# Kernel optimization log

Measured on AMD Instinct MI355X. Metric: run time of the kernel, lower is better.

Reference implementation:

```python
import jax, jax.numpy as jnp
import numpy as np

NEG_INF = -1.0e9  # matches the module's explicit -1e9 masking constant


def setup_inputs() -> dict:
    key = jax.random.key(0)
    B, T, D = 8, 2048, 1024
    x = jax.random.normal(key, (B, T, D), dtype=jnp.float32)
    return {"x": x}


def reference(x):
    # x: [B, T, D]
    T = x.shape[1]
    # raw QK^T scores: [B, T, T]
    scores = jnp.einsum('btd,bsd->bts', x, x)
    # torch.tril(scores, -1) + torch.triu(ones*-1e9, 0):
    # keep strictly-lower entries, set diagonal and upper to -1e9.
    strict_lower = jnp.tril(jnp.ones((T, T), dtype=bool), k=-1)
    scores = jnp.where(strict_lower, scores, jnp.float32(NEG_INF))
    # NOTE: row 0 is all -1e9 -> softmax yields uniform 1/T (faithful to the torch code).
    att_weights = jax.nn.softmax(scores, axis=-1)  # [B, T, T]
    att_vec = jnp.einsum('bts,bsd->btd', att_weights, x)  # [B, T, D]
    return att_vec, att_weights
```

## Files before the change

### kernel.cpp

```cpp
#include <hip/hip_runtime.h>

#define B_ 8
#define T_ 2048
#define D_ 1024

typedef __attribute__((ext_vector_type(8))) short bf16x8;
typedef __attribute__((ext_vector_type(8))) _Float16 f16x8;
typedef __attribute__((ext_vector_type(4))) float f32x4;
typedef __attribute__((ext_vector_type(8))) unsigned short u16x8;
typedef __attribute__((ext_vector_type(4))) unsigned short u16x4;

__device__ __forceinline__ unsigned short f2bf(float f) {
  union { float f; unsigned u; } v; v.f = f;
  unsigned r = v.u + 0x7FFFu + ((v.u >> 16) & 1u);
  return (unsigned short)(r >> 16);
}
__device__ __forceinline__ float bf2f(unsigned short h) {
  union { unsigned u; float f; } v; v.u = ((unsigned)h) << 16; return v.f;
}
__device__ __forceinline__ unsigned short f2h(float f) {
  union { _Float16 h; unsigned short u; } v; v.h = (_Float16)f; return v.u;
}

__device__ __forceinline__ void gl2lds16(const void* g, void* l) {
  __builtin_amdgcn_global_load_lds(
      (__attribute__((address_space(1))) void*)g,
      (__attribute__((address_space(3))) void*)l, 16, 0, 0);
}

__global__ __launch_bounds__(256) void prep_kernel(
    const float* __restrict__ x,
    unsigned short* __restrict__ xh, unsigned short* __restrict__ xl,
    unsigned short* __restrict__ xth) {
  const int b = blockIdx.z;
  const int t0 = blockIdx.y << 6;
  const int d0 = blockIdx.x << 6;
  __shared__ unsigned short tf[64][68];
  const int tid = threadIdx.x;
  const int r = tid >> 2, cq = tid & 3;
  const size_t xoff = ((size_t)b * T_ + t0 + r) * D_ + d0;
#pragma unroll
  for (int k = 0; k < 4; ++k) {
    const int col = (cq << 2) + (k << 4);
    const float4 v = *(const float4*)(x + xoff + col);
    const unsigned short h0 = f2bf(v.x), h1 = f2bf(v.y), h2 = f2bf(v.z), h3 = f2bf(v.w);
    const unsigned short l0 = f2bf(v.x - bf2f(h0)), l1 = f2bf(v.y - bf2f(h1));
    const unsigned short l2 = f2bf(v.z - bf2f(h2)), l3 = f2bf(v.w - bf2f(h3));
    u16x4 hv = {h0, h1, h2, h3}, lv = {l0, l1, l2, l3};
    *(u16x4*)(xh + xoff + col) = hv;
    *(u16x4*)(xl + xoff + col) = lv;
    tf[col + 0][r] = f2h(v.x); tf[col + 1][r] = f2h(v.y);
    tf[col + 2][r] = f2h(v.z); tf[col + 3][r] = f2h(v.w);
  }
  __syncthreads();
  const int dr = tid >> 2, tq = tid & 3;
  const size_t toff = ((size_t)b * D_ + d0 + dr) * T_ + t0;
#pragma unroll
  for (int c = 0; c < 2; ++c) {
    const int tcol = (tq << 3) + (c << 5);
    *(u16x8*)(xth + toff + tcol) = *(const u16x8*)&tf[dr][tcol];
  }
}

__global__ __launch_bounds__(256, 4) void scores_mfma(
    const unsigned short* __restrict__ xh, const unsigned short* __restrict__ xl,
    float* __restrict__ w) {
  const int id = blockIdx.x;
  const int sid = ((id & 7) * 136) + (id >> 3);
  const int b = sid / 136;
  const int L = sid - b * 136;
  int tt = (int)((sqrtf(8.f * (float)L + 1.f) - 1.f) * 0.5f);
  while (((tt + 1) * (tt + 2) >> 1) <= L) ++tt;
  while (((tt * (tt + 1)) >> 1) > L) --tt;
  const int ts = L - ((tt * (tt + 1)) >> 1);

  const int t0 = tt << 7, s0 = ts << 7;
  __shared__ unsigned short Ah[128 * 32];
  __shared__ unsigned short Al[128 * 32];
  __shared__ unsigned short Bh[128 * 32];
  __shared__ unsigned short Bl[128 * 32];
  const int tid = threadIdx.x;
  const int lane = tid & 63, wv = tid >> 6;
  const int wr = (wv >> 1) << 6, wc = (wv & 1) << 6;
  const int quad = lane >> 4, r16 = lane & 15;
  const int swz = ((quad ^ (r16 & 3) ^ ((r16 >> 2) & 1)) << 3);
  const size_t xb = (size_t)b * T_ * D_;

  f32x4 acc[4][4];
#pragma unroll
  for (int i = 0; i < 4; ++i)
#pragma unroll
    for (int j = 0; j < 4; ++j) acc[i][j] = (f32x4){0.f, 0.f, 0.f, 0.f};

  for (int k0 = 0; k0 < D_; k0 += 32) {
    __syncthreads();
#pragma unroll
    for (int i = 0; i < 2; ++i) {
      const int cc = (wv << 7) + (i << 6) + lane;
      const int row = cc >> 2, q = cc & 3;
      const int gq = q ^ (row & 3) ^ ((row >> 2) & 1);
      const int ldsoff = (((wv << 7) + (i << 6)) << 3);
      const size_t ga = xb + (size_t)(t0 + row) * D_ + k0 + (gq << 3);
      const size_t gb = xb + (size_t)(s0 + row) * D_ + k0 + (gq << 3);
      gl2lds16(xh + ga, &Ah[ldsoff]);
      gl2lds16(xl + ga, &Al[ldsoff]);
      gl2lds16(xh + gb, &Bh[ldsoff]);
      gl2lds16(xl + gb, &Bl[ldsoff]);
    }
    __syncthreads();
    bf16x8 ah[4], al[4];
#pragma unroll
    for (int i = 0; i < 4; ++i) {
      const int ra = ((wr + (i << 4) + r16) << 5) + swz;
      ah[i] = *(const bf16x8*)&Ah[ra];
      al[i] = *(const bf16x8*)&Al[ra];
    }
#pragma unroll
    for (int j = 0; j < 4; ++j) {
      const int rb = ((wc + (j << 4) + r16) << 5) + swz;
      const bf16x8 bhj = *(const bf16x8*)&Bh[rb];
      const bf16x8 blj = *(const bf16x8*)&Bl[rb];
#pragma unroll
      for (int i = 0; i < 4; ++i)
        acc[i][j] = __builtin_amdgcn_mfma_f32_16x16x32_bf16(ah[i], bhj, acc[i][j], 0, 0, 0);
#pragma unroll
      for (int i = 0; i < 4; ++i)
        acc[i][j] = __builtin_amdgcn_mfma_f32_16x16x32_bf16(ah[i], blj, acc[i][j], 0, 0, 0);
#pragma unroll
      for (int i = 0; i < 4; ++i)
        acc[i][j] = __builtin_amdgcn_mfma_f32_16x16x32_bf16(al[i], bhj, acc[i][j], 0, 0, 0);
    }
  }

  float* wb = w + (size_t)b * T_ * T_;
#pragma unroll
  for (int i = 0; i < 4; ++i)
#pragma unroll
    for (int j = 0; j < 4; ++j) {
      const int rr = t0 + wr + (i << 4) + (quad << 2);
      const int cc = s0 + wc + (j << 4) + r16;
#pragma unroll
      for (int rg = 0; rg < 4; ++rg)
        wb[(size_t)(rr + rg) * T_ + cc] = acc[i][j][rg];
    }
}

template <bool EMIT>
__global__ __launch_bounds__(256) void softmax_kernel(float* __restrict__ w,
                                                      unsigned short* __restrict__ wf) {
  const int row = (blockIdx.x << 2) + (threadIdx.x >> 6);
  const int t = row & (T_ - 1);
  const int lane = threadIdx.x & 63;
  float* wr = w + (size_t)row * T_;
  unsigned short* wfr = wf + (size_t)row * T_;

  if (t == 0) {
    const float u = 1.0f / 2048.0f;
    const float4 uv = {u, u, u, u};
#pragma unroll
    for (int k = 0; k < 8; ++k) *(float4*)&wr[(lane << 2) + (k << 8)] = uv;
    if (EMIT && lane < 32) {
      u16x4 z = {0, 0, 0, 0};
      *(u16x4*)&wfr[lane << 2] = z;
    }
    return;
  }

  float4 v[8];
  float m = -3.0e38f;
#pragma unroll
  for (int k = 0; k < 8; ++k) {
    const int s = (lane << 2) + (k << 8);
    float4 val = {-1.0e30f, -1.0e30f, -1.0e30f, -1.0e30f};
    if (s < t) {
      const float4 g = *(const float4*)&wr[s];
      val.x = g.x;
      val.y = (s + 1 < t) ? g.y : -1.0e30f;
      val.z = (s + 2 < t) ? g.z : -1.0e30f;
      val.w = (s + 3 < t) ? g.w : -1.0e30f;
    }
    v[k] = val;
    m = fmaxf(m, fmaxf(fmaxf(val.x, val.y), fmaxf(val.z, val.w)));
  }
#pragma unroll
  for (int off = 32; off; off >>= 1) m = fmaxf(m, __shfl_xor(m, off));

  float l = 0.f;
#pragma unroll
  for (int k = 0; k < 8; ++k) {
    v[k].x = __expf(v[k].x - m);
    v[k].y = __expf(v[k].y - m);
    v[k].z = __expf(v[k].z - m);
    v[k].w = __expf(v[k].w - m);
    l += (v[k].x + v[k].y) + (v[k].z + v[k].w);
  }
#pragma unroll
  for (int off = 32; off; off >>= 1) l += __shfl_xor(l, off);
  const float inv = 1.0f / l;

  const int smax_emit = ((t >> 7) + 1) << 7;
#pragma unroll
  for (int k = 0; k < 8; ++k) {
    const int s = (lane << 2) + (k << 8);
    const float4 o = {v[k].x * inv, v[k].y * inv, v[k].z * inv, v[k].w * inv};
    *(float4*)&wr[s] = o;
    if (EMIT && s < smax_emit) {
      u16x4 h = {f2h(o.x), f2h(o.y), f2h(o.z), f2h(o.w)};
      *(u16x4*)&wfr[s] = h;
    }
  }
}

template <bool USE_WF16>
__global__ __launch_bounds__(256, 4) void av_mfma(
    const float* __restrict__ w, const unsigned short* __restrict__ wf,
    const unsigned short* __restrict__ xth, float* __restrict__ out) {
  const int xid = blockIdx.x;
  const int td = xid >> 4;
  const int ti = xid & 15;
  const int tt = (ti < 8) ? ti : (23 - ti);
  const int b = blockIdx.z;
  const int t0 = tt << 7, d0 = td << 7;
  __shared__ unsigned short Aw[128 * 64];
  __shared__ unsigned short Bx[128 * 64];
  const int tid = threadIdx.x;
  const int lane = tid & 63, wv = tid >> 6;
  const int wr = (wv >> 1) << 6, wc = (wv & 1) << 6;
  const int quad = lane >> 4, r16 = lane & 15;
  const size_t xtb = (size_t)b * D_ * T_;
  const size_t wbase = (size_t)b * T_ * T_;
  const int smax = t0 + 128;

  f32x4 acc[4][4];
#pragma unroll
  for (int i = 0; i < 4; ++i)
#pragma unroll
    for (int j = 0; j < 4; ++j) acc[i][j] = (f32x4){0.f, 0.f, 0.f, 0.f};

  for (int s0 = 0; s0 < smax; s0 += 64) {
    __syncthreads();
    if (USE_WF16) {
#pragma unroll
      for (int i = 0; i < 4; ++i) {
        const int cc = (wv << 8) + (i << 6) + lane;
        const int rowa = cc >> 3, q = cc & 7;
        const int gq = q ^ (rowa & 7);
        const int ldsoff = (((wv << 8) + (i << 6)) << 3);
        gl2lds16(wf + wbase + (size_t)(t0 + rowa) * T_ + s0 + (gq << 3), &Aw[ldsoff]);
      }
    } else {
      const int rowa = tid >> 1, half = tid & 1;
      const float* g = w + wbase + (size_t)(t0 + rowa) * T_ + s0 + (half << 5);
      const int rs = rowa & 7;
#pragma unroll
      for (int p = 0; p < 4; ++p) {
        const float4 va = ((const float4*)g)[2 * p];
        const float4 vb = ((const float4*)g)[2 * p + 1];
        u16x8 pk = {f2h(va.x), f2h(va.y), f2h(va.z), f2h(va.w),
                    f2h(vb.x), f2h(vb.y), f2h(vb.z), f2h(vb.w)};
        const int c = (half << 2) + p;
        *(u16x8*)&Aw[(rowa << 6) + ((c ^ rs) << 3)] = pk;
      }
    }
#pragma unroll
    for (int i = 0; i < 4; ++i) {
      const int cc = (wv << 8) + (i << 6) + lane;
      const int rowb = cc >> 3, q = cc & 7;
      const int gq = q ^ (rowb & 7);
      const int ldsoff = (((wv << 8) + (i << 6)) << 3);
      gl2lds16(xth + xtb + (size_t)(d0 + rowb) * T_ + s0 + (gq << 3), &Bx[ldsoff]);
    }
    __syncthreads();
#pragma unroll
    for (int h = 0; h < 2; ++h) {
      f16x8 a[4];
#pragma unroll
      for (int i = 0; i < 4; ++i) {
        const int ar = wr + (i << 4) + r16;
        a[i] = *(const f16x8*)&Aw[(ar << 6) + ((((h << 2) | quad) ^ (ar & 7)) << 3)];
      }
#pragma unroll
      for (int j = 0; j < 4; ++j) {
        const int br = wc + (j << 4) + r16;
        const f16x8 bbj = *(const f16x8*)&Bx[(br << 6) + ((((h << 2) | quad) ^ (br & 7)) << 3)];
#pragma unroll
        for (int i = 0; i < 4; ++i)
          acc[i][j] = __builtin_amdgcn_mfma_f32_16x16x32_f16(a[i], bbj, acc[i][j], 0, 0, 0);
      }
    }
  }

  float* ob = out + (size_t)b * T_ * D_;
#pragma unroll
  for (int i = 0; i < 4; ++i)
#pragma unroll
    for (int j = 0; j < 4; ++j) {
      const int rr = t0 + wr + (i << 4) + (quad << 2);
      const int cc = d0 + wc + (j << 4) + r16;
#pragma unroll
      for (int rg = 0; rg < 4; ++rg)
        ob[(size_t)(rr + rg) * D_ + cc] = acc[i][j][rg];
    }
}

__global__ __launch_bounds__(256) void row0_partial(const float* __restrict__ x,
                                                    float* __restrict__ part) {
  const int tc = blockIdx.x, b = blockIdx.y;
  const int tid = threadIdx.x;
  const float* xb = x + ((size_t)b * T_ + (tc << 5)) * D_;
  float4 s = {0.f, 0.f, 0.f, 0.f};
#pragma unroll 4
  for (int r = 0; r < 32; ++r) {
    const float4 v = *(const float4*)(xb + (size_t)r * D_ + (tid << 2));
    s.x += v.x; s.y += v.y; s.z += v.z; s.w += v.w;
  }
  *(float4*)(part + ((size_t)((b << 6) + tc)) * D_ + (tid << 2)) = s;
}

__global__ __launch_bounds__(256) void row0_reduce(const float* __restrict__ part,
                                                   float* __restrict__ out) {
  const int b = blockIdx.x;
  const int tid = threadIdx.x;
  float4 s = {0.f, 0.f, 0.f, 0.f};
#pragma unroll 8
  for (int p = 0; p < 64; ++p) {
    const float4 v = *(const float4*)(part + ((size_t)((b << 6) + p)) * D_ + (tid << 2));
    s.x += v.x; s.y += v.y; s.z += v.z; s.w += v.w;
  }
  const float sc = 1.0f / 2048.0f;
  float4 o = {s.x * sc, s.y * sc, s.z * sc, s.w * sc};
  *(float4*)(out + (size_t)b * T_ * D_ + (tid << 2)) = o;
}

extern "C" void kernel_launch(void* const* d_in, const int* in_sizes, int n_in,
                              void* d_out, int out_size, void* d_ws, size_t ws_size,
                              hipStream_t stream) {
  const float* x = (const float*)d_in[0];
  float* att_vec = (float*)d_out;
  float* w = (float*)d_out + (size_t)B_ * T_ * D_;

  unsigned short* xh = (unsigned short*)att_vec;
  unsigned short* xl = xh + (size_t)B_ * T_ * D_;
  const size_t xthN = (size_t)B_ * D_ * T_;
  const size_t wfN = (size_t)B_ * T_ * T_;
  unsigned short* xth = (unsigned short*)d_ws;
  unsigned short* wf16 = xth + xthN;
  const size_t need = xthN * 2 + wfN * 2 + (size_t)512 * D_ * 4;
  const bool use_wf16 = (ws_size >= need);
  float* part = use_wf16 ? (float*)(wf16 + wfN) : (float*)(xth + xthN);

  prep_kernel<<<dim3(D_ / 64, T_ / 64, B_), 256, 0, stream>>>(x, xh, xl, xth);
  scores_mfma<<<dim3(8 * 136), 256, 0, stream>>>(xh, xl, w);
  if (use_wf16) {
    softmax_kernel<true><<<dim3(B_ * T_ / 4), 256, 0, stream>>>(w, wf16);
    av_mfma<true><<<dim3(128, 1, B_), 256, 0, stream>>>(w, wf16, xth, att_vec);
  } else {
    softmax_kernel<false><<<dim3(B_ * T_ / 4), 256, 0, stream>>>(w, wf16);
    av_mfma<false><<<dim3(128, 1, B_), 256, 0, stream>>>(w, wf16, xth, att_vec);
  }
  row0_partial<<<dim3(64, B_), 256, 0, stream>>>(x, part);
  row0_reduce<<<dim3(B_), 256, 0, stream>>>(part, att_vec);
}
```

Measured before the change: 505.6 us.

## Fuse row-0 column sums into prep, pair AV tiles, use nontemporal stores

```diff
diff --git a/kernel.cpp b/kernel.cpp
--- a/kernel.cpp
+++ b/kernel.cpp
@@ -21,6 +21,9 @@
 __device__ __forceinline__ unsigned short f2h(float f) {
   union { _Float16 h; unsigned short u; } v; v.h = (_Float16)f; return v.u;
 }
+__device__ __forceinline__ float h2f(unsigned short u) {
+  union { unsigned short u; _Float16 h; } v; v.u = u; return (float)v.h;
+}
 
 __device__ __forceinline__ void gl2lds16(const void* g, void* l) {
   __builtin_amdgcn_global_load_lds(
@@ -31,7 +34,7 @@
 __global__ __launch_bounds__(256) void prep_kernel(
     const float* __restrict__ x,
     unsigned short* __restrict__ xh, unsigned short* __restrict__ xl,
-    unsigned short* __restrict__ xth) {
+    unsigned short* __restrict__ xth, float* __restrict__ part) {
   const int b = blockIdx.z;
   const int t0 = blockIdx.y << 6;
   const int d0 = blockIdx.x << 6;
@@ -55,11 +58,19 @@
   __syncthreads();
   const int dr = tid >> 2, tq = tid & 3;
   const size_t toff = ((size_t)b * D_ + d0 + dr) * T_ + t0;
+  float cs = 0.f;
 #pragma unroll
   for (int c = 0; c < 2; ++c) {
     const int tcol = (tq << 3) + (c << 5);
-    *(u16x8*)(xth + toff + tcol) = *(const u16x8*)&tf[dr][tcol];
-  }
+    const u16x8 vv = *(const u16x8*)&tf[dr][tcol];
+    *(u16x8*)(xth + toff + tcol) = vv;
+#pragma unroll
+    for (int e = 0; e < 8; ++e) cs += h2f(vv[e]);
+  }
+  cs += __shfl_xor(cs, 1);
+  cs += __shfl_xor(cs, 2);
+  if (tq == 0)
+    part[(((size_t)b << 5) + blockIdx.y) * D_ + d0 + dr] = cs;
 }
 
 __global__ __launch_bounds__(256, 4) void scores_mfma(
@@ -156,9 +167,10 @@
 
   if (t == 0) {
     const float u = 1.0f / 2048.0f;
-    const float4 uv = {u, u, u, u};
-#pragma unroll
-    for (int k = 0; k < 8; ++k) *(float4*)&wr[(lane << 2) + (k << 8)] = uv;
+    const f32x4 uv = {u, u, u, u};
+#pragma unroll
+    for (int k = 0; k < 8; ++k)
+      __builtin_nontemporal_store(uv, (f32x4*)&wr[(lane << 2) + (k << 8)]);
     if (EMIT && lane < 32) {
       u16x4 z = {0, 0, 0, 0};
       *(u16x4*)&wfr[lane << 2] = z;
@@ -202,10 +214,10 @@
 #pragma unroll
   for (int k = 0; k < 8; ++k) {
     const int s = (lane << 2) + (k << 8);
-    const float4 o = {v[k].x * inv, v[k].y * inv, v[k].z * inv, v[k].w * inv};
-    *(float4*)&wr[s] = o;
+    const f32x4 o = {v[k].x * inv, v[k].y * inv, v[k].z * inv, v[k].w * inv};
+    __builtin_nontemporal_store(o, (f32x4*)&wr[s]);
     if (EMIT && s < smax_emit) {
-      u16x4 h = {f2h(o.x), f2h(o.y), f2h(o.z), f2h(o.w)};
+      u16x4 h = {f2h(o[0]), f2h(o[1]), f2h(o[2]), f2h(o[3])};
       *(u16x4*)&wfr[s] = h;
     }
   }
@@ -216,11 +228,10 @@
     const float* __restrict__ w, const unsigned short* __restrict__ wf,
     const unsigned short* __restrict__ xth, float* __restrict__ out) {
   const int xid = blockIdx.x;
-  const int td = xid >> 4;
-  const int ti = xid & 15;
-  const int tt = (ti < 8) ? ti : (23 - ti);
+  const int td = xid >> 3;
+  const int kp = xid & 7;
   const int b = blockIdx.z;
-  const int t0 = tt << 7, d0 = td << 7;
+  const int d0 = td << 7;
   __shared__ unsigned short Aw[128 * 64];
   __shared__ unsigned short Bx[128 * 64];
   const int tid = threadIdx.x;
@@ -229,92 +240,84 @@
   const int quad = lane >> 4, r16 = lane & 15;
   const size_t xtb = (size_t)b * D_ * T_;
   const size_t wbase = (size_t)b * T_ * T_;
-  const int smax = t0 + 128;
-
-  f32x4 acc[4][4];
-#pragma unroll
-  for (int i = 0; i < 4; ++i)
-#pragma unroll
-    for (int j = 0; j < 4; ++j) acc[i][j] = (f32x4){0.f, 0.f, 0.f, 0.f};
-
-  for (int s0 = 0; s0 < smax; s0 += 64) {
-    __syncthreads();
-    if (USE_WF16) {
+  float* ob = out + (size_t)b * T_ * D_;
+
+#pragma unroll 1
+  for (int mtile = 0; mtile < 2; ++mtile) {
+    const int tt = mtile ? (15 - kp) : kp;
+    const int t0 = tt << 7;
+    const int smax = t0 + 128;
+
+    f32x4 acc[4][4];
+#pragma unroll
+    for (int i = 0; i < 4; ++i)
+#pragma unroll
+      for (int j = 0; j < 4; ++j) acc[i][j] = (f32x4){0.f, 0.f, 0.f, 0.f};
+
+    for (int s0 = 0; s0 < smax; s0 += 64) {
+      __syncthreads();
+      if (USE_WF16) {
+#pragma unroll
+        for (int i = 0; i < 4; ++i) {
+          const int cc = (wv << 8) + (i << 6) + lane;
+          const int rowa = cc >> 3, q = cc & 7;
+          const int gq = q ^ (rowa & 7);
+          const int ldsoff = (((wv << 8) + (i << 6)) << 3);
+          gl2lds16(wf + wbase + (size_t)(t0 + rowa) * T_ + s0 + (gq << 3), &Aw[ldsoff]);
+        }
+      } else {
+        const int rowa = tid >> 1, half = tid & 1;
+        const float* g = w + wbase + (size_t)(t0 + rowa) * T_ + s0 + (half << 5);
+        const int rs = rowa & 7;
+#pragma unroll
+        for (int p = 0; p < 4; ++p) {
+          const float4 va = ((const float4*)g)[2 * p];
+          const float4 vb = ((const float4*)g)[2 * p + 1];
+          u16x8 pk = {f2h(va.x), f2h(va.y), f2h(va.z), f2h(va.w),
+                      f2h(vb.x), f2h(vb.y), f2h(vb.z), f2h(vb.w)};
+          const int c = (half << 2) + p;
+          *(u16x8*)&Aw[(rowa << 6) + ((c ^ rs) << 3)] = pk;
+        }
+      }
 #pragma unroll
       for (int i = 0; i < 4; ++i) {
         const int cc = (wv << 8) + (i << 6) + lane;
-        const int rowa = cc >> 3, q = cc & 7;
-        const int gq = q ^ (rowa & 7);
+        const int rowb = cc >> 3, q = cc & 7;
+        const int gq = q ^ (rowb & 7);
         const int ldsoff = (((wv << 8) + (i << 6)) << 3);
-        gl2lds16(wf + wbase + (size_t)(t0 + rowa) * T_ + s0 + (gq << 3), &Aw[ldsoff]);
+        gl2lds16(xth + xtb + (size_t)(d0 + rowb) * T_ + s0 + (gq << 3), &Bx[ldsoff]);
       }
-    } else {
-      const int rowa = tid >> 1, half = tid & 1;
-      const float* g = w + wbase + (size_t)(t0 + rowa) * T_ + s0 + (half << 5);
-      const int rs = rowa & 7;
-#pragma unroll
-      for (int p = 0; p < 4; ++p) {
-        const float4 va = ((const float4*)g)[2 * p];
-        const float4 vb = ((const float4*)g)[2 * p + 1];
-        u16x8 pk = {f2h(va.x), f2h(va.y), f2h(va.z), f2h(va.w),
-                    f2h(vb.x), f2h(vb.y), f2h(vb.z), f2h(vb.w)};
-        const int c = (half << 2) + p;
-        *(u16x8*)&Aw[(rowa << 6) + ((c ^ rs) << 3)] = pk;
+      __syncthreads();
+#pragma unroll
+      for (int h = 0; h < 2; ++h) {
+        f16x8 a[4];
+#pragma unroll
+        for (int i = 0; i < 4; ++i) {
+          const int ar = wr + (i << 4) + r16;
+          a[i] = *(const f16x8*)&Aw[(ar << 6) + ((((h << 2) | quad) ^ (ar & 7)) << 3)];
+        }
+#pragma unroll
+        for (int j = 0; j < 4; ++j) {
+          const int br = wc + (j << 4) + r16;
+          const f16x8 bbj = *(const f16x8*)&Bx[(br << 6) + ((((h << 2) | quad) ^ (br & 7)) << 3)];
+#pragma unroll
+          for (int i = 0; i < 4; ++i)
+            acc[i][j] = __builtin_amdgcn_mfma_f32_16x16x32_f16(a[i], bbj, acc[i][j], 0, 0, 0);
+        }
       }
     }
-#pragma unroll
-    for (int i = 0; i < 4; ++i) {
-      const int cc = (wv << 8) + (i << 6) + lane;
-      const int rowb = cc >> 3, q = cc & 7;
-      const int gq = q ^ (rowb & 7);
-      const int ldsoff = (((wv << 8) + (i << 6)) << 3);
-      gl2lds16(xth + xtb + (size_t)(d0 + rowb) * T_ + s0 + (gq << 3), &Bx[ldsoff]);
-    }
-    __syncthreads();
-#pragma unroll
-    for (int h = 0; h < 2; ++h) {
-      f16x8 a[4];
-#pragma unroll
-      for (int i = 0; i < 4; ++i) {
-        const int ar = wr + (i << 4) + r16;
-        a[i] = *(const f16x8*)&Aw[(ar << 6) + ((((h << 2) | quad) ^ (ar & 7)) << 3)];
+
+#pragma unroll
+    for (int i = 0; i < 4; ++i)
+#pragma unroll
+      for (int j = 0; j < 4; ++j) {
+        const int rr = t0 + wr + (i << 4) + (quad << 2);
+        const int cc = d0 + wc + (j << 4) + r16;
+#pragma unroll
+        for (int rg = 0; rg < 4; ++rg)
+          __builtin_nontemporal_store(acc[i][j][rg], &ob[(size_t)(rr + rg) * D_ + cc]);
       }
-#pragma unroll
-      for (int j = 0; j < 4; ++j) {
-        const int br = wc + (j << 4) + r16;
-        const f16x8 bbj = *(const f16x8*)&Bx[(br << 6) + ((((h << 2) | quad) ^ (br & 7)) << 3)];
-#pragma unroll
-        for (int i = 0; i < 4; ++i)
-          acc[i][j] = __builtin_amdgcn_mfma_f32_16x16x32_f16(a[i], bbj, acc[i][j], 0, 0, 0);
-      }
-    }
-  }
-
-  float* ob = out + (size_t)b * T_ * D_;
-#pragma unroll
-  for (int i = 0; i < 4; ++i)
-#pragma unroll
-    for (int j = 0; j < 4; ++j) {
-      const int rr = t0 + wr + (i << 4) + (quad << 2);
-      const int cc = d0 + wc + (j << 4) + r16;
-#pragma unroll
-      for (int rg = 0; rg < 4; ++rg)
-        ob[(size_t)(rr + rg) * D_ + cc] = acc[i][j][rg];
-    }
-}
-
-__global__ __launch_bounds__(256) void row0_partial(const float* __restrict__ x,
-                                                    float* __restrict__ part) {
-  const int tc = blockIdx.x, b = blockIdx.y;
-  const int tid = threadIdx.x;
-  const float* xb = x + ((size_t)b * T_ + (tc << 5)) * D_;
-  float4 s = {0.f, 0.f, 0.f, 0.f};
-#pragma unroll 4
-  for (int r = 0; r < 32; ++r) {
-    const float4 v = *(const float4*)(xb + (size_t)r * D_ + (tid << 2));
-    s.x += v.x; s.y += v.y; s.z += v.z; s.w += v.w;
-  }
-  *(float4*)(part + ((size_t)((b << 6) + tc)) * D_ + (tid << 2)) = s;
+  }
 }
 
 __global__ __launch_bounds__(256) void row0_reduce(const float* __restrict__ part,
@@ -323,8 +326,8 @@
   const int tid = threadIdx.x;
   float4 s = {0.f, 0.f, 0.f, 0.f};
 #pragma unroll 8
-  for (int p = 0; p < 64; ++p) {
-    const float4 v = *(const float4*)(part + ((size_t)((b << 6) + p)) * D_ + (tid << 2));
+  for (int p = 0; p < 32; ++p) {
+    const float4 v = *(const float4*)(part + (((size_t)b << 5) + p) * D_ + (tid << 2));
     s.x += v.x; s.y += v.y; s.z += v.z; s.w += v.w;
   }
   const float sc = 1.0f / 2048.0f;
@@ -345,19 +348,18 @@
   const size_t wfN = (size_t)B_ * T_ * T_;
   unsigned short* xth = (unsigned short*)d_ws;
   unsigned short* wf16 = xth + xthN;
-  const size_t need = xthN * 2 + wfN * 2 + (size_t)512 * D_ * 4;
+  const size_t need = xthN * 2 + wfN * 2 + (size_t)256 * D_ * 4;
   const bool use_wf16 = (ws_size >= need);
   float* part = use_wf16 ? (float*)(wf16 + wfN) : (float*)(xth + xthN);
 
-  prep_kernel<<<dim3(D_ / 64, T_ / 64, B_), 256, 0, stream>>>(x, xh, xl, xth);
+  prep_kernel<<<dim3(D_ / 64, T_ / 64, B_), 256, 0, stream>>>(x, xh, xl, xth, part);
   scores_mfma<<<dim3(8 * 136), 256, 0, stream>>>(xh, xl, w);
   if (use_wf16) {
     softmax_kernel<true><<<dim3(B_ * T_ / 4), 256, 0, stream>>>(w, wf16);
-    av_mfma<true><<<dim3(128, 1, B_), 256, 0, stream>>>(w, wf16, xth, att_vec);
+    av_mfma<true><<<dim3(64, 1, B_), 256, 0, stream>>>(w, wf16, xth, att_vec);
   } else {
     softmax_kernel<false><<<dim3(B_ * T_ / 4), 256, 0, stream>>>(w, wf16);
-    av_mfma<false><<<dim3(128, 1, B_), 256, 0, stream>>>(w, wf16, xth, att_vec);
-  }
-  row0_partial<<<dim3(64, B_), 256, 0, stream>>>(x, part);
+    av_mfma<false><<<dim3(64, 1, B_), 256, 0, stream>>>(w, wf16, xth, att_vec);
+  }
   row0_reduce<<<dim3(B_), 256, 0, stream>>>(part, att_vec);
 }
```

Result: faster. 468.6 us (-7.3%).
